# Kernel optimization log

Measured on AMD Instinct MI355X. Metric: run time of the kernel, lower is better.

## Reference

```python
import jax, jax.numpy as jnp
import numpy as np

L = 96   # num_layers per GRU stack == seq_len (required by h0 construction in source)
B = 128  # batch
T = 96   # seq_len
D = 3    # input features (x,y,z landmark coords)


def _u(key, shape, s):
    return jax.random.uniform(key, shape, jnp.float32, minval=-s, maxval=s)


def setup_inputs() -> dict:
    key = jax.random.key(0)
    ks = iter(jax.random.split(key, 40))
    inp = {"x": jax.random.normal(next(ks), (B, T, D), jnp.float32)}

    def gru_params(pfx, din, h):
        s = 1.0 / np.sqrt(h).astype(np.float32)  # PyTorch GRU init scale
        inp[pfx + "_wih0"] = _u(next(ks), (3 * h, din), s)   # layer 0 input weights
        inp[pfx + "_bih0"] = _u(next(ks), (3 * h,), s)
        inp[pfx + "_whh0"] = _u(next(ks), (3 * h, h), s)
        inp[pfx + "_bhh0"] = _u(next(ks), (3 * h,), s)
        inp[pfx + "_wih"] = _u(next(ks), (L - 1, 3 * h, h), s)  # layers 1..L-1 (input dim == h)
        inp[pfx + "_bih"] = _u(next(ks), (L - 1, 3 * h), s)
        inp[pfx + "_whh"] = _u(next(ks), (L - 1, 3 * h, h), s)
        inp[pfx + "_bhh"] = _u(next(ks), (L - 1, 3 * h), s)

    gru_params("g1", D, 64)
    gru_params("g2", 64, 128)
    gru_params("g3", 128, 64)

    inp["d1_w"] = _u(next(ks), (64, 64), 1.0 / 8)
    inp["d1_b"] = _u(next(ks), (64,), 1.0 / 8)
    inp["d2_w"] = _u(next(ks), (32, 64), 1.0 / 8)
    inp["d2_b"] = _u(next(ks), (32,), 1.0 / 8)
    inp["d3_w"] = _u(next(ks), (250, 32), 1.0 / np.sqrt(32).astype(np.float32))
    inp["d3_b"] = _u(next(ks), (250,), 1.0 / np.sqrt(32).astype(np.float32))
    return inp


def _gru_layer(x, wih, bih, whh, bhh):
    # x: [B,T,Din]; wih: [3H,Din]; whh: [3H,H]. PyTorch gate order: r,z,n.
    h = whh.shape[1]
    xg = jnp.einsum('btd,gd->btg', x, wih) + bih  # precompute input gates [B,T,3H]

    def step(hprev, xg_t):
        hg = hprev @ whh.T + bhh
        xr, xz, xn = jnp.split(xg_t, 3, axis=-1)
        hr, hz, hn = jnp.split(hg, 3, axis=-1)
        r = jax.nn.sigmoid(xr + hr)
        z = jax.nn.sigmoid(xz + hz)
        n = jnp.tanh(xn + r * hn)
        hnew = (1.0 - z) * n + z * hprev
        return hnew, hnew

    h0 = jnp.zeros((x.shape[0], h), x.dtype)
    _, ys = jax.lax.scan(step, h0, jnp.swapaxes(xg, 0, 1))  # scan over time
    return jnp.swapaxes(ys, 0, 1)  # [B,T,H]


def _gru_stack(x, wih0, bih0, whh0, bhh0, wih, bih, whh, bhh):
    y = _gru_layer(x, wih0, bih0, whh0, bhh0)

    def body(y, p):
        return _gru_layer(y, p[0], p[1], p[2], p[3]), None

    y, _ = jax.lax.scan(body, y, (wih, bih, whh, bhh))  # scan over layers 1..L-1
    return y


def reference(x,
              g1_wih0, g1_bih0, g1_whh0, g1_bhh0, g1_wih, g1_bih, g1_whh, g1_bhh,
              g2_wih0, g2_bih0, g2_whh0, g2_bhh0, g2_wih, g2_bih, g2_whh, g2_bhh,
              g3_wih0, g3_bih0, g3_whh0, g3_bhh0, g3_wih, g3_bih, g3_whh, g3_bhh,
              d1_w, d1_b, d2_w, d2_b, d3_w, d3_b):
    y = _gru_stack(x, g1_wih0, g1_bih0, g1_whh0, g1_bhh0, g1_wih, g1_bih, g1_whh, g1_bhh)
    y = _gru_stack(y, g2_wih0, g2_bih0, g2_whh0, g2_bhh0, g2_wih, g2_bih, g2_whh, g2_bhh)
    y = _gru_stack(y, g3_wih0, g3_bih0, g3_whh0, g3_bhh0, g3_wih, g3_bih, g3_whh, g3_bhh)
    h = y[:, -1, :]  # last timestep [B,64]
    h = jax.nn.relu(h @ d1_w.T + d1_b)
    h = jax.nn.relu(h @ d2_w.T + d2_b)
    return jax.nn.relu(h @ d3_w.T + d3_b)  # [B,250]
```

## Files before the change

### kernel.cpp

```cpp
#include <hip/hip_runtime.h>


#define TPB 512
#define DRING 4
#define FS 64
#define PROBE_A 0x51CAFE77
#define PROBE_B 0x2B2B2B2B

typedef float vf4 __attribute__((ext_vector_type(4)));

__device__ __forceinline__ float sigmoid_f(float x) { return 1.0f / (1.0f + __expf(-x)); }
__device__ __forceinline__ float tanh_f(float x)    { return 1.0f - 2.0f / (__expf(2.0f * x) + 1.0f); }

__device__ __forceinline__ int cp_load(const int* p) {
    return __hip_atomic_load(p, __ATOMIC_RELAXED, __HIP_MEMORY_SCOPE_AGENT);
}
__device__ __forceinline__ void cp_store(int* p, int v) {
    __hip_atomic_store(p, v, __ATOMIC_RELAXED, __HIP_MEMORY_SCOPE_AGENT);
}
__device__ __forceinline__ int cp_poll_nz(const int* p) {
    int v;
    while (!(v = cp_load(p))) __builtin_amdgcn_s_sleep(8);
    return v;
}

__device__ __forceinline__ void vmwait0() { asm volatile("s_waitcnt vmcnt(0)" ::: "memory"); }
__device__ __forceinline__ int ld_l2_b32_wait(const int* p) {
    int r;
    asm volatile("global_load_dword %0, %1, off sc0\n\t"
                 "s_waitcnt vmcnt(0)"
                 : "=v"(r) : "v"(p) : "memory");
    return r;
}
__device__ __forceinline__ void st_l2_b32(int* p, int v) {
    asm volatile("global_store_dword %0, %1, off sc0" :: "v"(p), "v"(v) : "memory");
}
__device__ __forceinline__ void st_l2_f4(float* p, float4 v) {
    vf4 w; w[0] = v.x; w[1] = v.y; w[2] = v.z; w[3] = v.w;
    asm volatile("global_store_dwordx4 %0, %1, off sc0" :: "v"(p), "v"(w) : "memory");
}
__device__ __forceinline__ void ld_l2_2xf4(const float* p0, const float* p1,
                                           vf4& a, vf4& b) {
    asm volatile("global_load_dwordx4 %0, %2, off sc0\n\t"
                 "global_load_dwordx4 %1, %3, off sc0\n\t"
                 "s_waitcnt vmcnt(0)"
                 : "=&v"(a), "=&v"(b)
                 : "v"(p0), "v"(p1)
                 : "memory");
}
__device__ __forceinline__ void ld_l2_4xf4(const float* p0, const float* p1,
                                           const float* p2, const float* p3,
                                           vf4& a, vf4& b, vf4& c, vf4& d) {
    asm volatile("global_load_dwordx4 %0, %4, off sc0\n\t"
                 "global_load_dwordx4 %1, %5, off sc0\n\t"
                 "global_load_dwordx4 %2, %6, off sc0\n\t"
                 "global_load_dwordx4 %3, %7, off sc0\n\t"
                 "s_waitcnt vmcnt(0)"
                 : "=&v"(a), "=&v"(b), "=&v"(c), "=&v"(d)
                 : "v"(p0), "v"(p1), "v"(p2), "v"(p3)
                 : "memory");
}

__device__ __forceinline__ void st_cp_f4(float* p, float4 v) {
    vf4 w; w[0] = v.x; w[1] = v.y; w[2] = v.z; w[3] = v.w;
    asm volatile("global_store_dwordx4 %0, %1, off sc0 sc1" :: "v"(p), "v"(w) : "memory");
}
__device__ __forceinline__ void ld_cp_2xf4(const float* p0, const float* p1,
                                           vf4& a, vf4& b) {
    asm volatile("global_load_dwordx4 %0, %2, off sc0 sc1\n\t"
                 "global_load_dwordx4 %1, %3, off sc0 sc1\n\t"
                 "s_waitcnt vmcnt(0)"
                 : "=&v"(a), "=&v"(b)
                 : "v"(p0), "v"(p1)
                 : "memory");
}
__device__ __forceinline__ void ld_cp_4xf4(const float* p0, const float* p1,
                                           const float* p2, const float* p3,
                                           vf4& a, vf4& b, vf4& c, vf4& d) {
    asm volatile("global_load_dwordx4 %0, %4, off sc0 sc1\n\t"
                 "global_load_dwordx4 %1, %5, off sc0 sc1\n\t"
                 "global_load_dwordx4 %2, %6, off sc0 sc1\n\t"
                 "global_load_dwordx4 %3, %7, off sc0 sc1\n\t"
                 "s_waitcnt vmcnt(0)"
                 : "=&v"(a), "=&v"(b), "=&v"(c), "=&v"(d)
                 : "v"(p0), "v"(p1), "v"(p2), "v"(p3)
                 : "memory");
}

__device__ __forceinline__ void wait_flag(int* fp, int tgt, bool fast) {
    if (fast) { while (ld_l2_b32_wait(fp) < tgt) __builtin_amdgcn_s_sleep(1); }
    else      { while (cp_load(fp) < tgt)        __builtin_amdgcn_s_sleep(2); }
}

struct PassArgs {
    const float* wih0; const float* bih0; const float* whh0; const float* bhh0;
    const float* wihA; const float* bihA; const float* whhA; const float* bhhA;
    int firstLayer;
    int NL;
    const float* seqIn;
    long seqTs;
    float* seqOut;
    float* hFinal;
    float* rings;
    int* done;
    int* prb;
    const float* xg;
};

template<int STACK>
__global__ __launch_bounds__(TPB, 2) void pass_kernel(PassArgs A)
{
    constexpr int NG    = (STACK == 2) ? 96 : 192;
    constexpr int NB    = (STACK == 2) ? 128 : 64;
    constexpr int KH    = (STACK == 2) ? 128 : 64;
    constexpr int KI    = (STACK == 2) ? 128 : 64;
    constexpr int PARTS = (STACK == 2) ? 4 : 2;
    constexpr int JS    = NG / 3;
    constexpr int NGG   = NG / 6;
    constexpr int WROW  = NGG * 12;
    constexpr int XGT   = (STACK == 2) ? 384 * 128 : 192 * 128;

    __shared__ __align__(16) float wt_hh[(KH / 2) * WROW];
    __shared__ __align__(16) float wt_ih[(KI / 2) * WROW];
    __shared__ __align__(16) float atile[64 * NB];
    __shared__ __align__(16) float hbuf[64 * 64];

    const int tid  = threadIdx.x;

    const int bidx = blockIdx.x;
    int l, part;
    if (STACK == 2) { l = 6  * (bidx & 7) + ((bidx >> 3) >> 2); part = (bidx >> 3) & 3; }
    else            { l = 12 * (bidx & 7) + ((bidx >> 3) >> 1); part = (bidx >> 3) & 1; }
    const int rb = l * PARTS + part;
    const int gl = A.firstLayer + l;

    const int gg = tid & (NGG - 1);
    const int bg = tid / NGG;
    const int jl0 = 2 * gg, jl1 = 2 * gg + 1;
    const int b0 = 4 * bg;

    const float *wih, *bih, *whh, *bhh;
    if (gl == 0) { wih = A.wih0; bih = A.bih0; whh = A.whh0; bhh = A.bhh0; }
    else {
        const int wsz = (STACK == 2) ? 384 * 128 : 192 * 64;
        const int bs  = (STACK == 2) ? 384 : 192;
        wih = A.wihA + (size_t)(gl - 1) * wsz; bih = A.bihA + (size_t)(gl - 1) * bs;
        whh = A.whhA + (size_t)(gl - 1) * wsz; bhh = A.bhhA + (size_t)(gl - 1) * bs;
    }

    auto grow = [&](int r) -> int {
        if (STACK == 2) return (r >> 5) * 128 + 32 * part + (r & 31);
        return r;
    };

    for (int i = tid; i < NG * KH; i += TPB) {
        int r = i / KH, k = i - r * KH;
        int g = r / JS, j = r - g * JS;
        wt_hh[(k >> 1) * WROW + (j >> 1) * 12 + (k & 1) * 6 + g * 2 + (j & 1)]
            = whh[(size_t)grow(r) * KH + k];
    }
    if (l > 0) {
        for (int i = tid; i < NG * KI; i += TPB) {
            int r = i / KI, k = i - r * KI;
            int g = r / JS, j = r - g * JS;
            wt_ih[(k >> 1) * WROW + (j >> 1) * 12 + (k & 1) * 6 + g * 2 + (j & 1)]
                = wih[(size_t)grow(r) * KI + k];
        }
    }

    float bR[2], bZ[2], bNH[2], bNI[2];
#pragma unroll
    for (int jj = 0; jj < 2; ++jj) {
        int jl = jl0 + jj;
        bR[jj]  = bhh[grow(jl)]          + bih[grow(jl)];
        bZ[jj]  = bhh[grow(JS + jl)]     + bih[grow(JS + jl)];
        bNH[jj] = bhh[grow(2 * JS + jl)];
        bNI[jj] = bih[grow(2 * JS + jl)];
    }

    float hprev[2][4];
#pragma unroll
    for (int jj = 0; jj < 2; ++jj)
#pragma unroll
        for (int bb = 0; bb < 4; ++bb) hprev[jj][bb] = 0.0f;

    bool f_in = false, f_out = false, f_fl_self = false, f_fl_par = false, f_fl_child = false;
    {
        int* hsk = (int*)atile;
        const int NL = A.NL;
        if (STACK != 2) {
            if (tid == 0 && l < NL - 1) {
                int* rg = A.prb + (size_t)rb * FS;
                cp_store(rg, PROBE_A); vmwait0();
                (void)ld_l2_b32_wait(rg);
                cp_store(rg, PROBE_B); vmwait0();
                cp_store(rg + 1, 1);
            }
            if (tid == 1 && l > 0) {
                int* rg = A.prb + (size_t)((l - 1) * PARTS + part) * FS;
                (void)cp_poll_nz(rg + 1);
                int v = ld_l2_b32_wait(rg);
                cp_store(rg + 2, (v == PROBE_A) ? 2 : 1);
            }
            if (tid >= 8 && tid < 12) {
                int j = l - 2 + (tid - 8);
                hsk[tid - 8] = (j >= 0 && j < NL - 1)
                    ? cp_poll_nz(A.prb + (size_t)(j * PARTS + part) * FS + 2) : 0;
            }
        } else {
            if (part == 0 && tid < 4 && (tid > 0 || l < NL - 1)) {
                int* rg = A.prb + (size_t)(l * 4 + tid) * FS;
                cp_store(rg, PROBE_A); vmwait0();
                (void)ld_l2_b32_wait(rg);
                cp_store(rg, PROBE_B); vmwait0();
                cp_store(rg + 1, 1);
            }
            if (tid == 4 && (part != 0 || l > 0)) {
                int* rg = (part != 0) ? A.prb + (size_t)(l * 4 + part) * FS
                                      : A.prb + (size_t)((l - 1) * 4) * FS;
                (void)cp_poll_nz(rg + 1);
                int v = ld_l2_b32_wait(rg);
                cp_store(rg + 2, (v == PROBE_A) ? 2 : 1);
            }
            if (tid >= 8 && tid < 28) {
                int q = tid - 8, r = q >> 2, p = q & 3;
                int a = l - 2 + r;
                bool valid = (a >= 0 && a < NL) && (p > 0 || a < NL - 1);
                hsk[q] = valid ? cp_poll_nz(A.prb + (size_t)(a * 4 + p) * FS + 2) : 0;
            }
        }
        __syncthreads();
        if (STACK != 2) {
            const int NLl = A.NL;
            bool pp0 = hsk[0] == 2, pp1 = hsk[1] == 2, pp2 = hsk[2] == 2, pp3 = hsk[3] == 2;
            f_in       = (l > 0) && pp1;
            f_out      = (l == NLl - 1) || pp2;
            f_fl_self  = (l == 0 || pp1) && (l == NLl - 1 || pp2);
            f_fl_par   = (l > 0) && pp1 && (l < 2 || pp0);
            f_fl_child = (l < NLl - 1) && pp2 && (l + 2 >= NLl || pp3);
        } else {
            const int NLl = A.NL;
            bool S[5], T[4];
#pragma unroll
            for (int r = 0; r < 5; ++r)
                S[r] = hsk[r * 4 + 1] == 2 && hsk[r * 4 + 2] == 2 && hsk[r * 4 + 3] == 2;
#pragma unroll
            for (int r = 0; r < 4; ++r) T[r] = hsk[r * 4 + 0] == 2;
            f_out      = S[2] && (l == NLl - 1 || (S[3] && T[2]));
            f_in       = (l > 0) && S[1] && S[2] && T[1];
            f_fl_self  = S[2] && (l == 0 || (S[1] && T[1])) && (l == NLl - 1 || (S[3] && T[2]));
            f_fl_par   = (l > 0) && S[1] && S[2] && T[1] && (l < 2 || (S[0] && T[0]));
            f_fl_child = (l < NLl - 1) && S[2] && S[3] && T[2] && (l + 2 >= NLl || (S[4] && T[3]));
        }
        __syncthreads();
    }

    auto gemmP = [&](const float* wt, const float* at, int astride,
                     float (&accR)[2][4], float (&accZ)[2][4], float (&accN)[2][4]) {
#pragma unroll 2
        for (int k2 = 0; k2 < 32; ++k2) {
            const float* wr = wt + k2 * WROW + gg * 12;
            vf4 q0 = *(const vf4*)(wr);
            vf4 q1 = *(const vf4*)(wr + 4);
            vf4 q2 = *(const vf4*)(wr + 8);
            const float* ar = at + (2 * k2) * astride + b0;
            float4 a0v = *(const float4*)(ar);
            float4 a1v = *(const float4*)(ar + astride);
            float a0[4] = {a0v.x, a0v.y, a0v.z, a0v.w};
            float a1[4] = {a1v.x, a1v.y, a1v.z, a1v.w};
#pragma unroll
            for (int bb = 0; bb < 4; ++bb) {
                accR[0][bb] += q0.x * a0[bb];  accR[1][bb] += q0.y * a0[bb];
                accZ[0][bb] += q0.z * a0[bb];  accZ[1][bb] += q0.w * a0[bb];
                accN[0][bb] += q1.x * a0[bb];  accN[1][bb] += q1.y * a0[bb];
                accR[0][bb] += q1.z * a1[bb];  accR[1][bb] += q1.w * a1[bb];
                accZ[0][bb] += q2.x * a1[bb];  accZ[1][bb] += q2.y * a1[bb];
                accN[0][bb] += q2.z * a1[bb];  accN[1][bb] += q2.w * a1[bb];
            }
        }
    };

    auto stage2 = [&](int baseBlk, int slotT, int kt, bool fast) {
        const float* p[4];
#pragma unroll
        for (int q = 0; q < 4; ++q) {
            int u4 = tid + q * TPB, r = u4 >> 5, c4 = u4 & 31, kk = kt * 64 + r;
            p[q] = A.rings + ((size_t)(baseBlk + (kk >> 5)) * DRING + slotT) * 4096
                           + (kk & 31) * 128 + 4 * c4;
        }
        vf4 ta, tb, tc, td;
        if (fast) ld_l2_4xf4(p[0], p[1], p[2], p[3], ta, tb, tc, td);
        else      ld_cp_4xf4(p[0], p[1], p[2], p[3], ta, tb, tc, td);
        {
            int u4, r, c4;
            u4 = tid;           r = u4 >> 5; c4 = u4 & 31; *(vf4*)&atile[r * 128 + 4 * c4] = ta;
            u4 = tid + TPB;     r = u4 >> 5; c4 = u4 & 31; *(vf4*)&atile[r * 128 + 4 * c4] = tb;
            u4 = tid + 2 * TPB; r = u4 >> 5; c4 = u4 & 31; *(vf4*)&atile[r * 128 + 4 * c4] = tc;
            u4 = tid + 3 * TPB; r = u4 >> 5; c4 = u4 & 31; *(vf4*)&atile[r * 128 + 4 * c4] = td;
        }
    };

    for (int t = 0; t < 96; ++t) {
        float accR[2][4] = {}, accZ[2][4] = {}, accNH[2][4] = {}, accNI[2][4] = {};

        if (STACK != 2) {
            if (t > 0) gemmP(wt_hh, hbuf, 64, accR, accZ, accNH);

            if (tid < 8) {
                int grp = tid >> 2, idx = tid & 3;
                int* fp = nullptr; int tgt = 0; bool fm = false;
                if (grp == 0) { if (l > 0 && idx == part)
                                { fp = &A.done[((l - 1) * PARTS + idx) * FS]; tgt = t + 1; fm = f_fl_par; } }
                else          { if (t >= DRING && l < A.NL - 1 && idx == part)
                                { fp = &A.done[((l + 1) * PARTS + idx) * FS]; tgt = t - DRING + 1; fm = f_fl_child; } }
                if (fp) wait_flag(fp, tgt, fm);
            }
            __syncthreads();

            if (l == 0) {
                const float* xgp = A.xg + (size_t)t * XGT + 64 * part + b0;
                auto xgacc = [&](int row, float (&acc)[4]) {
                    float4 xv = *(const float4*)&xgp[(size_t)row * 128];
                    acc[0] += xv.x; acc[1] += xv.y; acc[2] += xv.z; acc[3] += xv.w;
                };
                xgacc(jl0, accR[0]);            xgacc(jl1, accR[1]);
                xgacc(JS + jl0, accZ[0]);       xgacc(JS + jl1, accZ[1]);
                xgacc(2 * JS + jl0, accNI[0]);  xgacc(2 * JS + jl1, accNI[1]);
            } else {
                const float* slot = A.rings + ((size_t)((l - 1) * PARTS + part) * DRING + (t & 3)) * 4096;
                vf4 ta, tb;
                if (f_in) ld_l2_2xf4(slot + 4 * tid, slot + 4 * (tid + TPB), ta, tb);
                else      ld_cp_2xf4(slot + 4 * tid, slot + 4 * (tid + TPB), ta, tb);
                *(vf4*)&atile[4 * tid] = ta;
                *(vf4*)&atile[4 * (tid + TPB)] = tb;
                __syncthreads();
                gemmP(wt_ih, atile, 64, accR, accZ, accNI);
            }
        } else {
            if (t > 0) {
                if (tid < 4 && tid != part)
                    wait_flag(&A.done[(l * 4 + tid) * FS], t, f_fl_self);
                __syncthreads();
                for (int kt = 0; kt < 2; ++kt) {
                    if (kt) __syncthreads();
                    stage2(l * 4, (t - 1) & 3, kt, f_out);
                    __syncthreads();
                    gemmP(wt_hh + kt * 32 * WROW, atile, 128, accR, accZ, accNH);
                }
            }

            if (tid < 8) {
                int grp = tid >> 2, idx = tid & 3;
                int* fp = nullptr; int tgt = 0; bool fm = false;
                if (grp == 0) { if (l > 0) { fp = &A.done[((l - 1) * 4 + idx) * FS]; tgt = t + 1; fm = f_fl_par; } }
                else          { if (t >= DRING && l < A.NL - 1)
                                { fp = &A.done[((l + 1) * 4 + idx) * FS]; tgt = t - DRING + 1; fm = f_fl_child; } }
                if (fp) wait_flag(fp, tgt, fm);
            }
            __syncthreads();

            if (l == 0) {
                const float* xgp = A.xg + (size_t)t * XGT + b0;
                auto xgacc = [&](int row, float (&acc)[4]) {
                    float4 xv = *(const float4*)&xgp[(size_t)row * 128];
                    acc[0] += xv.x; acc[1] += xv.y; acc[2] += xv.z; acc[3] += xv.w;
                };
                xgacc(grow(jl0), accR[0]);            xgacc(grow(jl1), accR[1]);
                xgacc(grow(JS + jl0), accZ[0]);       xgacc(grow(JS + jl1), accZ[1]);
                xgacc(grow(2 * JS + jl0), accNI[0]);  xgacc(grow(2 * JS + jl1), accNI[1]);
            } else {
                for (int kt = 0; kt < 2; ++kt) {
                    if (kt) __syncthreads();
                    stage2((l - 1) * 4, t & 3, kt, f_in);
                    __syncthreads();
                    gemmP(wt_ih + kt * 32 * WROW, atile, 128, accR, accZ, accNI);
                }
            }
        }

        float4 hv[2];
#pragma unroll
        for (int jj = 0; jj < 2; ++jj) {
            float* hp = (float*)&hv[jj];
#pragma unroll
            for (int bb = 0; bb < 4; ++bb) {
                float r = sigmoid_f(accR[jj][bb] + bR[jj]);
                float z = sigmoid_f(accZ[jj][bb] + bZ[jj]);
                float n = tanh_f(accNI[jj][bb] + bNI[jj] + r * (accNH[jj][bb] + bNH[jj]));
                float h = (1.0f - z) * n + z * hprev[jj][bb];
                hprev[jj][bb] = h;
                hp[bb] = h;
            }
        }
        float* slot = A.rings + ((size_t)rb * DRING + (t & 3)) * 4096;
        if (STACK == 2) {
            if (f_out) {
                st_l2_f4(&slot[jl0 * 128 + b0], hv[0]);
                st_l2_f4(&slot[jl1 * 128 + b0], hv[1]);
            } else {
                st_cp_f4(&slot[jl0 * 128 + b0], hv[0]);
                st_cp_f4(&slot[jl1 * 128 + b0], hv[1]);
            }
            if (A.seqOut && l == A.NL - 1) {
                *(float4*)&A.seqOut[(size_t)t * 16384 + (32 * part + jl0) * 128 + b0] = hv[0];
                *(float4*)&A.seqOut[(size_t)t * 16384 + (32 * part + jl1) * 128 + b0] = hv[1];
            }
        } else {
            if (f_out) {
                st_l2_f4(&slot[jl0 * 64 + b0], hv[0]);
                st_l2_f4(&slot[jl1 * 64 + b0], hv[1]);
            } else {
                st_cp_f4(&slot[jl0 * 64 + b0], hv[0]);
                st_cp_f4(&slot[jl1 * 64 + b0], hv[1]);
            }
            *(float4*)&hbuf[jl0 * 64 + b0] = hv[0];
            *(float4*)&hbuf[jl1 * 64 + b0] = hv[1];
            if (A.seqOut && l == A.NL - 1) {
                *(float4*)&A.seqOut[(size_t)t * 16384 + jl0 * 128 + 64 * part + b0] = hv[0];
                *(float4*)&A.seqOut[(size_t)t * 16384 + jl1 * 128 + 64 * part + b0] = hv[1];
            }
            if (STACK == 3 && l == A.NL - 1 && t == 95 && A.hFinal) {
                *(float4*)&A.hFinal[jl0 * 128 + 64 * part + b0] = hv[0];
                *(float4*)&A.hFinal[jl1 * 128 + 64 * part + b0] = hv[1];
            }
        }
        vmwait0();
        __syncthreads();
        if (tid == 0) {
            if (f_fl_self) st_l2_b32(&A.done[rb * FS], t + 1);
            else           cp_store(&A.done[rb * FS], t + 1);
        }
    }
}

__global__ __launch_bounds__(256) void xg_kernel(const float* __restrict__ W,
    const float* __restrict__ X, float* __restrict__ XG,
    int NGtot, int din, long xts)
{
    __shared__ float xs[16384];
    const int t = blockIdx.x, r0 = blockIdx.y * 64, tid = threadIdx.x;
    for (int i = tid; i < din * 128; i += 256)
        xs[i] = X[(size_t)t * xts + i];
    __syncthreads();
    const int rr = tid >> 2, bq = tid & 3;
    const int r = r0 + rr;
    vf4 acc[8];
#pragma unroll
    for (int j = 0; j < 8; ++j) acc[j] = (vf4){0.f, 0.f, 0.f, 0.f};
    for (int k = 0; k < din; ++k) {
        float w = W[(size_t)r * din + k];
        const float* xr = &xs[k * 128 + bq * 32];
#pragma unroll
        for (int j = 0; j < 8; ++j) {
            vf4 xv = *(const vf4*)(xr + 4 * j);
            acc[j] += w * xv;
        }
    }
    float* out = &XG[((size_t)t * NGtot + r) * 128 + bq * 32];
#pragma unroll
    for (int j = 0; j < 8; ++j) *(vf4*)(out + 4 * j) = acc[j];
}

__global__ void xprep_kernel(const float* __restrict__ x, float* __restrict__ seqA)
{
    int i = blockIdx.x * 256 + threadIdx.x;
    if (i < 128 * 96 * 3) {
        int b = i / 288, r = i - b * 288;
        int t = r / 3, k = r - 3 * t;
        seqA[(size_t)t * 8192 + k * 128 + b] = x[i];
    }
}

__global__ __launch_bounds__(256) void head_kernel(
    const float* __restrict__ hF,
    const float* __restrict__ d1w, const float* __restrict__ d1b,
    const float* __restrict__ d2w, const float* __restrict__ d2b,
    const float* __restrict__ d3w, const float* __restrict__ d3b,
    float* __restrict__ out)
{
    const int b = blockIdx.x, tid = threadIdx.x;
    __shared__ float h1[64], h2[32];
    if (tid < 64) {
        float s = d1b[tid];
        for (int k = 0; k < 64; ++k) s += d1w[tid * 64 + k] * hF[k * 128 + b];
        h1[tid] = fmaxf(s, 0.0f);
    }
    __syncthreads();
    if (tid < 32) {
        float s = d2b[tid];
        for (int k = 0; k < 64; ++k) s += d2w[tid * 64 + k] * h1[k];
        h2[tid] = fmaxf(s, 0.0f);
    }
    __syncthreads();
    if (tid < 250) {
        float s = d3b[tid];
        for (int k = 0; k < 32; ++k) s += d3w[tid * 32 + k] * h2[k];
        out[b * 250 + tid] = fmaxf(s, 0.0f);
    }
}

extern "C" void kernel_launch(void* const* d_in, const int* in_sizes, int n_in,
                              void* d_out, int out_size, void* d_ws, size_t ws_size,
                              hipStream_t stream)
{
    const float* x       = (const float*)d_in[0];
    const float* g1_wih0 = (const float*)d_in[1];  const float* g1_bih0 = (const float*)d_in[2];
    const float* g1_whh0 = (const float*)d_in[3];  const float* g1_bhh0 = (const float*)d_in[4];
    const float* g1_wih  = (const float*)d_in[5];  const float* g1_bih  = (const float*)d_in[6];
    const float* g1_whh  = (const float*)d_in[7];  const float* g1_bhh  = (const float*)d_in[8];
    const float* g2_wih0 = (const float*)d_in[9];  const float* g2_bih0 = (const float*)d_in[10];
    const float* g2_whh0 = (const float*)d_in[11]; const float* g2_bhh0 = (const float*)d_in[12];
    const float* g2_wih  = (const float*)d_in[13]; const float* g2_bih  = (const float*)d_in[14];
    const float* g2_whh  = (const float*)d_in[15]; const float* g2_bhh  = (const float*)d_in[16];
    const float* g3_wih0 = (const float*)d_in[17]; const float* g3_bih0 = (const float*)d_in[18];
    const float* g3_whh0 = (const float*)d_in[19]; const float* g3_bhh0 = (const float*)d_in[20];
    const float* g3_wih  = (const float*)d_in[21]; const float* g3_bih  = (const float*)d_in[22];
    const float* g3_whh  = (const float*)d_in[23]; const float* g3_bhh  = (const float*)d_in[24];
    const float* d1w = (const float*)d_in[25]; const float* d1b = (const float*)d_in[26];
    const float* d2w = (const float*)d_in[27]; const float* d2b = (const float*)d_in[28];
    const float* d3w = (const float*)d_in[29]; const float* d3b = (const float*)d_in[30];

    float* wsf = (float*)d_ws;
    const size_t RINGS = (size_t)192 * DRING * 4096;
    const size_t B1SZ  = (size_t)96 * 128 * 128;
    const size_t SEQA  = (size_t)96 * 64 * 128;
    const int    SLOTN = 192 * FS;
    float* rings  = wsf;
    float* B1     = rings + RINGS;
    float* B2     = B1 + B1SZ;
    float* seqA   = B2 + B1SZ;
    float* hFinal = seqA + SEQA;
    int*   flags  = (int*)(hFinal + 8192);
    int*   prb    = flags + (size_t)4 * SLOTN;
    float* XG     = (float*)(prb + (size_t)4 * SLOTN);

    size_t zero_bytes = (B1SZ * 2 + SEQA + 8192) * sizeof(float)
                      + (size_t)8 * SLOTN * sizeof(int);
    (void)hipMemsetAsync(B1, 0, zero_bytes, stream);

    xprep_kernel<<<dim3(144), dim3(256), 0, stream>>>(x, seqA);

    PassArgs P;
    xg_kernel<<<dim3(96, 3), dim3(256), 0, stream>>>(g1_wih0, seqA, XG, 192, 3, 8192);
    P = {g1_wih0, g1_bih0, g1_whh0, g1_bhh0, g1_wih, g1_bih, g1_whh, g1_bhh,
         0, 96, seqA, 8192, B1, nullptr, rings, flags + 0 * SLOTN, prb + 0 * SLOTN, XG};
    pass_kernel<1><<<dim3(192), dim3(TPB), 0, stream>>>(P);

    xg_kernel<<<dim3(96, 6), dim3(256), 0, stream>>>(g2_wih0, B1, XG, 384, 64, 16384);
    P = {g2_wih0, g2_bih0, g2_whh0, g2_bhh0, g2_wih, g2_bih, g2_whh, g2_bhh,
         0, 48, B1, 16384, B2, nullptr, rings, flags + 1 * SLOTN, prb + 1 * SLOTN, XG};
    pass_kernel<2><<<dim3(192), dim3(TPB), 0, stream>>>(P);

    xg_kernel<<<dim3(96, 6), dim3(256), 0, stream>>>(g2_wih + (size_t)47 * 384 * 128, B2, XG,
                                                     384, 128, 16384);
    P = {g2_wih0, g2_bih0, g2_whh0, g2_bhh0, g2_wih, g2_bih, g2_whh, g2_bhh,
         48, 48, B2, 16384, B1, nullptr, rings, flags + 2 * SLOTN, prb + 2 * SLOTN, XG};
    pass_kernel<2><<<dim3(192), dim3(TPB), 0, stream>>>(P);

    xg_kernel<<<dim3(96, 3), dim3(256), 0, stream>>>(g3_wih0, B1, XG, 192, 128, 16384);
    P = {g3_wih0, g3_bih0, g3_whh0, g3_bhh0, g3_wih, g3_bih, g3_whh, g3_bhh,
         0, 96, B1, 16384, nullptr, hFinal, rings, flags + 3 * SLOTN, prb + 3 * SLOTN, XG};
    pass_kernel<3><<<dim3(192), dim3(TPB), 0, stream>>>(P);

    head_kernel<<<dim3(128), dim3(256), 0, stream>>>(hFinal, d1w, d1b, d2w, d2b, d3w, d3b,
                                                     (float*)d_out);
}
```

Baseline: 9.297 ms.

## Prefetch parent-layer ring slot asynchronously while computing recurrent GEMM

Moves all dependency-flag waits ahead of the timestep's compute and issues the input-ring loads as non-blocking global loads before the hidden-state GEMM. The loads then land in LDS after that GEMM, so their latency overlaps useful work. In the 128-wide stack the self-wait and the parent/child waits now run in parallel on separate threads instead of in two phases. In exchange, the hidden GEMM can no longer start before the parent flag arrives, and the vmwait relies on the compiler not placing other pending loads in between.

```diff
diff --git a/kernel.cpp b/kernel.cpp
--- a/kernel.cpp
+++ b/kernel.cpp
@@ -82,6 +82,45 @@
                  "global_load_dwordx4 %2, %6, off sc0 sc1\n\t"
                  "global_load_dwordx4 %3, %7, off sc0 sc1\n\t"
                  "s_waitcnt vmcnt(0)"
+                 : "=&v"(a), "=&v"(b), "=&v"(c), "=&v"(d)
+                 : "v"(p0), "v"(p1), "v"(p2), "v"(p3)
+                 : "memory");
+}
+
+__device__ __forceinline__ void ld_l2_2xf4_async(const float* p0, const float* p1,
+                                                 vf4& a, vf4& b) {
+    asm volatile("global_load_dwordx4 %0, %2, off sc0\n\t"
+                 "global_load_dwordx4 %1, %3, off sc0"
+                 : "=&v"(a), "=&v"(b)
+                 : "v"(p0), "v"(p1)
+                 : "memory");
+}
+__device__ __forceinline__ void ld_cp_2xf4_async(const float* p0, const float* p1,
+                                                 vf4& a, vf4& b) {
+    asm volatile("global_load_dwordx4 %0, %2, off sc0 sc1\n\t"
+                 "global_load_dwordx4 %1, %3, off sc0 sc1"
+                 : "=&v"(a), "=&v"(b)
+                 : "v"(p0), "v"(p1)
+                 : "memory");
+}
+__device__ __forceinline__ void ld_l2_4xf4_async(const float* p0, const float* p1,
+                                                 const float* p2, const float* p3,
+                                                 vf4& a, vf4& b, vf4& c, vf4& d) {
+    asm volatile("global_load_dwordx4 %0, %4, off sc0\n\t"
+                 "global_load_dwordx4 %1, %5, off sc0\n\t"
+                 "global_load_dwordx4 %2, %6, off sc0\n\t"
+                 "global_load_dwordx4 %3, %7, off sc0"
+                 : "=&v"(a), "=&v"(b), "=&v"(c), "=&v"(d)
+                 : "v"(p0), "v"(p1), "v"(p2), "v"(p3)
+                 : "memory");
+}
+__device__ __forceinline__ void ld_cp_4xf4_async(const float* p0, const float* p1,
+                                                 const float* p2, const float* p3,
+                                                 vf4& a, vf4& b, vf4& c, vf4& d) {
+    asm volatile("global_load_dwordx4 %0, %4, off sc0 sc1\n\t"
+                 "global_load_dwordx4 %1, %5, off sc0 sc1\n\t"
+                 "global_load_dwordx4 %2, %6, off sc0 sc1\n\t"
+                 "global_load_dwordx4 %3, %7, off sc0 sc1"
                  : "=&v"(a), "=&v"(b), "=&v"(c), "=&v"(d)
                  : "v"(p0), "v"(p1), "v"(p2), "v"(p3)
                  : "memory");
@@ -280,32 +319,32 @@
         }
     };
 
+    auto stage2_addr = [&](int baseBlk, int slotT, int kt, int q) -> const float* {
+        int u4 = tid + q * TPB, r = u4 >> 5, c4 = u4 & 31, kk = kt * 64 + r;
+        return A.rings + ((size_t)(baseBlk + (kk >> 5)) * DRING + slotT) * 4096
+                       + (kk & 31) * 128 + 4 * c4;
+    };
+    auto stage2_land = [&](vf4 ta, vf4 tb, vf4 tc, vf4 td) {
+        int u4, r, c4;
+        u4 = tid;           r = u4 >> 5; c4 = u4 & 31; *(vf4*)&atile[r * 128 + 4 * c4] = ta;
+        u4 = tid + TPB;     r = u4 >> 5; c4 = u4 & 31; *(vf4*)&atile[r * 128 + 4 * c4] = tb;
+        u4 = tid + 2 * TPB; r = u4 >> 5; c4 = u4 & 31; *(vf4*)&atile[r * 128 + 4 * c4] = tc;
+        u4 = tid + 3 * TPB; r = u4 >> 5; c4 = u4 & 31; *(vf4*)&atile[r * 128 + 4 * c4] = td;
+    };
     auto stage2 = [&](int baseBlk, int slotT, int kt, bool fast) {
         const float* p[4];
 #pragma unroll
-        for (int q = 0; q < 4; ++q) {
-            int u4 = tid + q * TPB, r = u4 >> 5, c4 = u4 & 31, kk = kt * 64 + r;
-            p[q] = A.rings + ((size_t)(baseBlk + (kk >> 5)) * DRING + slotT) * 4096
-                           + (kk & 31) * 128 + 4 * c4;
-        }
+        for (int q = 0; q < 4; ++q) p[q] = stage2_addr(baseBlk, slotT, kt, q);
         vf4 ta, tb, tc, td;
         if (fast) ld_l2_4xf4(p[0], p[1], p[2], p[3], ta, tb, tc, td);
         else      ld_cp_4xf4(p[0], p[1], p[2], p[3], ta, tb, tc, td);
-        {
-            int u4, r, c4;
-            u4 = tid;           r = u4 >> 5; c4 = u4 & 31; *(vf4*)&atile[r * 128 + 4 * c4] = ta;
-            u4 = tid + TPB;     r = u4 >> 5; c4 = u4 & 31; *(vf4*)&atile[r * 128 + 4 * c4] = tb;
-            u4 = tid + 2 * TPB; r = u4 >> 5; c4 = u4 & 31; *(vf4*)&atile[r * 128 + 4 * c4] = tc;
-            u4 = tid + 3 * TPB; r = u4 >> 5; c4 = u4 & 31; *(vf4*)&atile[r * 128 + 4 * c4] = td;
-        }
+        stage2_land(ta, tb, tc, td);
     };
 
     for (int t = 0; t < 96; ++t) {
         float accR[2][4] = {}, accZ[2][4] = {}, accNH[2][4] = {}, accNI[2][4] = {};
 
         if (STACK != 2) {
-            if (t > 0) gemmP(wt_hh, hbuf, 64, accR, accZ, accNH);
-
             if (tid < 8) {
                 int grp = tid >> 2, idx = tid & 3;
                 int* fp = nullptr; int tgt = 0; bool fm = false;
@@ -314,6 +353,23 @@
                 else          { if (t >= DRING && l < A.NL - 1 && idx == part)
                                 { fp = &A.done[((l + 1) * PARTS + idx) * FS]; tgt = t - DRING + 1; fm = f_fl_child; } }
                 if (fp) wait_flag(fp, tgt, fm);
+            }
+            __syncthreads();
+
+            vf4 s0, s1;
+            const bool stg = (l > 0);
+            if (stg) {
+                const float* slot = A.rings + ((size_t)((l - 1) * PARTS + part) * DRING + (t & 3)) * 4096;
+                if (f_in) ld_l2_2xf4_async(slot + 4 * tid, slot + 4 * (tid + TPB), s0, s1);
+                else      ld_cp_2xf4_async(slot + 4 * tid, slot + 4 * (tid + TPB), s0, s1);
+            }
+
+            if (t > 0) gemmP(wt_hh, hbuf, 64, accR, accZ, accNH);
+
+            if (stg) {
+                vmwait0();
+                *(vf4*)&atile[4 * tid] = s0;
+                *(vf4*)&atile[4 * (tid + TPB)] = s1;
             }
             __syncthreads();
 
@@ -327,20 +383,32 @@
                 xgacc(JS + jl0, accZ[0]);       xgacc(JS + jl1, accZ[1]);
                 xgacc(2 * JS + jl0, accNI[0]);  xgacc(2 * JS + jl1, accNI[1]);
             } else {
-                const float* slot = A.rings + ((size_t)((l - 1) * PARTS + part) * DRING + (t & 3)) * 4096;
-                vf4 ta, tb;
-                if (f_in) ld_l2_2xf4(slot + 4 * tid, slot + 4 * (tid + TPB), ta, tb);
-                else      ld_cp_2xf4(slot + 4 * tid, slot + 4 * (tid + TPB), ta, tb);
-                *(vf4*)&atile[4 * tid] = ta;
-                *(vf4*)&atile[4 * (tid + TPB)] = tb;
-                __syncthreads();
                 gemmP(wt_ih, atile, 64, accR, accZ, accNI);
             }
         } else {
+            if (t > 0 && tid < 4 && tid != part)
+                wait_flag(&A.done[(l * 4 + tid) * FS], t, f_fl_self);
+            if (tid >= 8 && tid < 16) {
+                int grp = (tid - 8) >> 2, idx = tid & 3;
+                int* fp = nullptr; int tgt = 0; bool fm = false;
+                if (grp == 0) { if (l > 0) { fp = &A.done[((l - 1) * 4 + idx) * FS]; tgt = t + 1; fm = f_fl_par; } }
+                else          { if (t >= DRING && l < A.NL - 1)
+                                { fp = &A.done[((l + 1) * 4 + idx) * FS]; tgt = t - DRING + 1; fm = f_fl_child; } }
+                if (fp) wait_flag(fp, tgt, fm);
+            }
+            __syncthreads();
+
+            vf4 e0, e1, e2, e3;
+            const bool pih = (l > 0);
+            if (pih) {
+                const float* p[4];
+#pragma unroll
+                for (int q = 0; q < 4; ++q) p[q] = stage2_addr((l - 1) * 4, t & 3, 0, q);
+                if (f_in) ld_l2_4xf4_async(p[0], p[1], p[2], p[3], e0, e1, e2, e3);
+                else      ld_cp_4xf4_async(p[0], p[1], p[2], p[3], e0, e1, e2, e3);
+            }
+
             if (t > 0) {
-                if (tid < 4 && tid != part)
-                    wait_flag(&A.done[(l * 4 + tid) * FS], t, f_fl_self);
-                __syncthreads();
                 for (int kt = 0; kt < 2; ++kt) {
                     if (kt) __syncthreads();
                     stage2(l * 4, (t - 1) & 3, kt, f_out);
@@ -348,16 +416,6 @@
                     gemmP(wt_hh + kt * 32 * WROW, atile, 128, accR, accZ, accNH);
                 }
             }
-
-            if (tid < 8) {
-                int grp = tid >> 2, idx = tid & 3;
-                int* fp = nullptr; int tgt = 0; bool fm = false;
-                if (grp == 0) { if (l > 0) { fp = &A.done[((l - 1) * 4 + idx) * FS]; tgt = t + 1; fm = f_fl_par; } }
-                else          { if (t >= DRING && l < A.NL - 1)
-                                { fp = &A.done[((l + 1) * 4 + idx) * FS]; tgt = t - DRING + 1; fm = f_fl_child; } }
-                if (fp) wait_flag(fp, tgt, fm);
-            }
-            __syncthreads();
 
             if (l == 0) {
                 const float* xgp = A.xg + (size_t)t * XGT + b0;
@@ -369,12 +427,15 @@
                 xgacc(grow(JS + jl0), accZ[0]);       xgacc(grow(JS + jl1), accZ[1]);
                 xgacc(grow(2 * JS + jl0), accNI[0]);  xgacc(grow(2 * JS + jl1), accNI[1]);
             } else {
-                for (int kt = 0; kt < 2; ++kt) {
-                    if (kt) __syncthreads();
-                    stage2((l - 1) * 4, t & 3, kt, f_in);
-                    __syncthreads();
-                    gemmP(wt_ih + kt * 32 * WROW, atile, 128, accR, accZ, accNI);
-                }
+                __syncthreads();
+                vmwait0();
+                stage2_land(e0, e1, e2, e3);
+                __syncthreads();
+                gemmP(wt_ih, atile, 128, accR, accZ, accNI);
+                __syncthreads();
+                stage2((l - 1) * 4, t & 3, 1, f_in);
+                __syncthreads();
+                gemmP(wt_ih + 32 * WROW, atile, 128, accR, accZ, accNI);
             }
         }
 
```

After: 11.36 ms. 1.22x slower.
